# Optimization experiments

Measured on AMD Instinct MI355X. Metric: run time of the kernel, lower is better.

## Reference

```python
import jax, jax.numpy as jnp
import numpy as np

C = 32          # mid_channel / in_channel
B = 8           # batch size (number of scenes)
N = 2_000_000   # total points across batch
BN_EPS = 1e-4   # BatchNorm1d eps from norm_fn


def setup_inputs() -> dict:
    key = jax.random.key(0)
    ks = jax.random.split(key, 8)
    s = 0.05
    return {
        "feats": jax.random.normal(ks[0], (N, C), dtype=jnp.float32),
        "batch_idxs": jnp.sort(jax.random.randint(ks[1], (N,), 0, B, dtype=jnp.int32)),
        "off_w1": jax.random.normal(ks[2], (C, C), dtype=jnp.float32) * s,
        "off_b1": jnp.zeros((C,), jnp.float32),
        "bn_gamma": jnp.ones((C,), jnp.float32),   # set_bn_init fills 1.0
        "bn_beta": jnp.zeros((C,), jnp.float32),   # set_bn_init fills 0.0
        "off_w2": jax.random.normal(ks[3], (C, 3), dtype=jnp.float32) * s,
        "off_b2": jnp.zeros((3,), jnp.float32),
        "mask_w1": jax.random.normal(ks[4], (C, C), dtype=jnp.float32) * s,
        "mask_b1": jnp.zeros((C,), jnp.float32),
        "mask_w2": jax.random.normal(ks[5], (C, 1), dtype=jnp.float32) * s,
        "mask_b2": jnp.zeros((1,), jnp.float32),
        "iou_w": jax.random.normal(ks[6], (C, 1), dtype=jnp.float32) * s,
        "iou_b": jnp.zeros((1,), jnp.float32),
    }


def reference(feats, batch_idxs, off_w1, off_b1, bn_gamma, bn_beta, off_w2, off_b2,
              mask_w1, mask_b1, mask_w2, mask_b2, iou_w, iou_b):
    # offset_linear = MLP([C, C, 3], norm_fn=BatchNorm1d): Linear -> BN -> ReLU -> Linear
    h = feats @ off_w1 + off_b1                      # [N, C]
    mu = h.mean(axis=0)
    var = jnp.mean(jnp.square(h - mu), axis=0)       # biased var (torch BN training fwd)
    h = (h - mu) * jax.lax.rsqrt(var + BN_EPS) * bn_gamma + bn_beta
    h = jax.nn.relu(h)
    pt_offsets = h @ off_w2 + off_b2                 # [N, 3]

    # mask_linear = MLP([C, C, 1], norm_fn=None): Linear -> ReLU -> Linear
    m = jax.nn.relu(feats @ mask_w1 + mask_b1)       # [N, C]
    mask_scores = m @ mask_w2 + mask_b2              # [N, 1]

    # global_pool: scatter mean of features over per-batch segments (batch offsets)
    ones = jnp.ones((feats.shape[0],), feats.dtype)
    counts = jax.ops.segment_sum(ones, batch_idxs, num_segments=B)          # [B]
    pooled = jax.ops.segment_sum(feats, batch_idxs, num_segments=B)         # [B, C]
    pooled = pooled / jnp.maximum(counts, 1.0)[:, None]

    # iou_score_linear on the pooled proposal feature
    iou_scores = pooled @ iou_w + iou_b              # [B, 1]
    return pt_offsets, mask_scores, pooled, iou_scores
```

## Files before the change

kernel.cpp:

```cpp
#include <hip/hip_runtime.h>

#define TPB 256

typedef __attribute__((ext_vector_type(8))) short short8;
typedef __attribute__((ext_vector_type(4))) float floatx4;

__device__ __forceinline__ unsigned short bf_rne(float f){
    union { float f; unsigned u; } c; c.f = f;
    unsigned r = c.u + 0x7fffu + ((c.u >> 16) & 1u);
    return (unsigned short)(r >> 16);
}
__device__ __forceinline__ unsigned pack_bf(float lo, float hi){
    union { float f; unsigned u; } a, b; a.f = lo; b.f = hi;
    return __builtin_amdgcn_perm(b.u, a.u, 0x07060302u);
}

__global__ void lb_kernel(const int* __restrict__ bidx, int* __restrict__ ws_lb,
                          int N, int B)
{
    const int t = threadIdx.x;
    if (t <= B){
        int lo = 0, hi = N;
        while (lo < hi){
            const int mid = (lo + hi) >> 1;
            if (bidx[mid] < t) lo = mid + 1; else hi = mid;
        }
        ws_lb[t] = lo;
    }
}

__global__ __launch_bounds__(TPB) void pass1_kernel(
    const float* __restrict__ feats, const int* __restrict__ ws_lb,
    const float* __restrict__ w1, const float* __restrict__ b1,
    const float* __restrict__ mw1, const float* __restrict__ mb1,
    const float* __restrict__ mw2, const float* __restrict__ mb2,
    float* __restrict__ mask_out,
    float* __restrict__ ws_sum, float* __restrict__ ws_sq,
    float* __restrict__ ws_pool, int N, int B)
{
    __shared__ float s_stage[TPB/64][1024];
    __shared__ float s_pool[8][32];
    __shared__ float s_sum[32];
    __shared__ float s_sq[32];
    __shared__ int   s_lb[9];

    const int tid  = threadIdx.x;
    const int lane = tid & 63;
    const int wv   = tid >> 6;
    const int p = lane & 15;
    const int q = lane >> 4;

    if (tid < 32){ s_sum[tid] = 0.f; s_sq[tid] = 0.f; }
    ((float*)s_pool)[tid] = 0.f;
    if (tid <= B) s_lb[tid] = ws_lb[tid];
    __syncthreads();

    short8 aw0, aw1, am0, am1;
    floatx4 ci_h0, ci_h1, ci_m0, ci_m1;
    float mw2v[8];
#pragma unroll
    for (int j = 0; j < 8; ++j){
        const int k = q * 8 + j;
        aw0[j] = (short)bf_rne(w1 [k * 32 + p]);
        aw1[j] = (short)bf_rne(w1 [k * 32 + 16 + p]);
        am0[j] = (short)bf_rne(mw1[k * 32 + p]);
        am1[j] = (short)bf_rne(mw1[k * 32 + 16 + p]);
    }
#pragma unroll
    for (int r = 0; r < 4; ++r){
        const int c0 = q * 4 + r, c1 = 16 + q * 4 + r;
        ci_h0[r] = b1[c0];  ci_h1[r] = b1[c1];
        ci_m0[r] = mb1[c0]; ci_m1[r] = mb1[c1];
        mw2v[r] = mw2[c0];  mw2v[4 + r] = mw2[c1];
    }
    const float mb2s = mb2[0];

    float hsum[8] = {0,0,0,0,0,0,0,0};
    float hsq [8] = {0,0,0,0,0,0,0,0};
    float pacc[4] = {0,0,0,0};

    const int ngroups = (N + 31) >> 5;
    const int nw  = gridDim.x * (TPB / 64);
    const int wid = blockIdx.x * (TPB / 64) + wv;
    const int g0  = (int)((long)wid       * ngroups / nw);
    const int gE  = (int)((long)(wid + 1) * ngroups / nw);

    int curb = 0;
    { const int r = g0 << 5; while (curb < B - 1 && r >= s_lb[curb + 1]) curb++; }
    int lbn = s_lb[curb + 1];

    float* sw = &s_stage[wv][0];
    const int wrow  = lane >> 3;
    const int wg    = (lane & 7) ^ wrow;
    const int cbase = (lane & 7) << 2;
    const int wo0 = ( 0 + wrow) * 32 + (wg << 2);
    const int wo1 = ( 8 + wrow) * 32 + (wg << 2);
    const int wo2 = (16 + wrow) * 32 + (wg << 2);
    const int wo3 = (24 + wrow) * 32 + (wg << 2);
    const int e = p & 7;
    const int ra0 = p * 32        + ((((q << 1)    ) ^ e) << 2);
    const int ra1 = p * 32        + ((((q << 1) + 1) ^ e) << 2);
    const int rb0 = (16 + p) * 32 + ((((q << 1)    ) ^ e) << 2);
    const int rb1 = (16 + p) * 32 + ((((q << 1) + 1) ^ e) << 2);

    floatx4 sv0 = {0,0,0,0}, sv1 = {0,0,0,0}, sv2 = {0,0,0,0}, sv3 = {0,0,0,0};
    if (g0 < gE){
        const float* gp = feats + ((size_t)g0 << 10) + (lane << 2);
        const int r = (g0 << 5) + wrow;
        if (r + 24 < N){
            sv0 = *(const floatx4*)(gp);
            sv1 = *(const floatx4*)(gp + 256);
            sv2 = *(const floatx4*)(gp + 512);
            sv3 = *(const floatx4*)(gp + 768);
        } else {
            if (r      < N) sv0 = *(const floatx4*)(gp);
            if (r +  8 < N) sv1 = *(const floatx4*)(gp + 256);
            if (r + 16 < N) sv2 = *(const floatx4*)(gp + 512);
            if (r + 24 < N) sv3 = *(const floatx4*)(gp + 768);
        }
    }

    for (int g = g0; g < gE; ++g){
        *(floatx4*)(sw + wo0) = sv0;
        *(floatx4*)(sw + wo1) = sv1;
        *(floatx4*)(sw + wo2) = sv2;
        *(floatx4*)(sw + wo3) = sv3;

        floatx4 nv0 = {0,0,0,0}, nv1 = {0,0,0,0}, nv2 = {0,0,0,0}, nv3 = {0,0,0,0};
        if (g + 1 < gE){
            const float* gp = feats + ((size_t)(g + 1) << 10) + (lane << 2);
            const int r = ((g + 1) << 5) + wrow;
            if (r + 24 < N){
                nv0 = *(const floatx4*)(gp);
                nv1 = *(const floatx4*)(gp + 256);
                nv2 = *(const floatx4*)(gp + 512);
                nv3 = *(const floatx4*)(gp + 768);
            } else {
                if (r      < N) nv0 = *(const floatx4*)(gp);
                if (r +  8 < N) nv1 = *(const floatx4*)(gp + 256);
                if (r + 16 < N) nv2 = *(const floatx4*)(gp + 512);
                if (r + 24 < N) nv3 = *(const floatx4*)(gp + 768);
            }
        }

        const int r0 = g << 5;
        if (r0 >= lbn){
#pragma unroll
            for (int j = 0; j < 4; ++j){
                if (pacc[j] != 0.f) atomicAdd(&s_pool[curb][cbase + j], pacc[j]);
                pacc[j] = 0.f;
            }
            do { curb++; } while (curb < B - 1 && r0 >= s_lb[curb + 1]);
            lbn = s_lb[curb + 1];
        }
        const bool slow = (r0 + 31 >= lbn) || (r0 + 31 >= N);

        if (!slow){
            pacc[0] += sv0[0] + sv1[0] + sv2[0] + sv3[0];
            pacc[1] += sv0[1] + sv1[1] + sv2[1] + sv3[1];
            pacc[2] += sv0[2] + sv1[2] + sv2[2] + sv3[2];
            pacc[3] += sv0[3] + sv1[3] + sv2[3] + sv3[3];
        } else {
#define SLOWROW(SV, L) { \
            const int row = r0 + (L * 8) + wrow; \
            if (row < N){ \
                int bl = curb; \
                for (int c = curb + 1; c < B; ++c) bl += (row >= s_lb[c]); \
                atomicAdd(&s_pool[bl][cbase + 0], SV[0]); \
                atomicAdd(&s_pool[bl][cbase + 1], SV[1]); \
                atomicAdd(&s_pool[bl][cbase + 2], SV[2]); \
                atomicAdd(&s_pool[bl][cbase + 3], SV[3]); \
            } }
            SLOWROW(sv0, 0) SLOWROW(sv1, 1) SLOWROW(sv2, 2) SLOWROW(sv3, 3)
#undef SLOWROW
        }

        const floatx4 vA0 = *(const floatx4*)(sw + ra0);
        const floatx4 vA1 = *(const floatx4*)(sw + ra1);
        const floatx4 vB0 = *(const floatx4*)(sw + rb0);
        const floatx4 vB1 = *(const floatx4*)(sw + rb1);

        short8 bfA, bfB;
        {
            unsigned* ba = (unsigned*)&bfA;
            ba[0] = pack_bf(vA0[0], vA0[1]); ba[1] = pack_bf(vA0[2], vA0[3]);
            ba[2] = pack_bf(vA1[0], vA1[1]); ba[3] = pack_bf(vA1[2], vA1[3]);
            unsigned* bb = (unsigned*)&bfB;
            bb[0] = pack_bf(vB0[0], vB0[1]); bb[1] = pack_bf(vB0[2], vB0[3]);
            bb[2] = pack_bf(vB1[0], vB1[1]); bb[3] = pack_bf(vB1[2], vB1[3]);
        }

        const floatx4 chA0 = __builtin_amdgcn_mfma_f32_16x16x32_bf16(aw0, bfA, ci_h0, 0, 0, 0);
        const floatx4 chA1 = __builtin_amdgcn_mfma_f32_16x16x32_bf16(aw1, bfA, ci_h1, 0, 0, 0);
        const floatx4 cmA0 = __builtin_amdgcn_mfma_f32_16x16x32_bf16(am0, bfA, ci_m0, 0, 0, 0);
        const floatx4 cmA1 = __builtin_amdgcn_mfma_f32_16x16x32_bf16(am1, bfA, ci_m1, 0, 0, 0);
        const floatx4 chB0 = __builtin_amdgcn_mfma_f32_16x16x32_bf16(aw0, bfB, ci_h0, 0, 0, 0);
        const floatx4 chB1 = __builtin_amdgcn_mfma_f32_16x16x32_bf16(aw1, bfB, ci_h1, 0, 0, 0);
        const floatx4 cmB0 = __builtin_amdgcn_mfma_f32_16x16x32_bf16(am0, bfB, ci_m0, 0, 0, 0);
        const floatx4 cmB1 = __builtin_amdgcn_mfma_f32_16x16x32_bf16(am1, bfB, ci_m1, 0, 0, 0);

        if (r0 + 31 < N){
#pragma unroll
            for (int r = 0; r < 4; ++r){
                const float a0 = chA0[r], b0 = chB0[r];
                hsum[r] += a0 + b0;
                hsq [r] = fmaf(a0, a0, fmaf(b0, b0, hsq[r]));
                const float a1 = chA1[r], b1v = chB1[r];
                hsum[4 + r] += a1 + b1v;
                hsq [4 + r] = fmaf(a1, a1, fmaf(b1v, b1v, hsq[4 + r]));
            }
        } else {
            if (r0 + p < N){
#pragma unroll
                for (int r = 0; r < 4; ++r){
                    const float a0 = chA0[r]; hsum[r]     += a0; hsq[r]     = fmaf(a0, a0, hsq[r]);
                    const float a1 = chA1[r]; hsum[4 + r] += a1; hsq[4 + r] = fmaf(a1, a1, hsq[4 + r]);
                }
            }
            if (r0 + 16 + p < N){
#pragma unroll
                for (int r = 0; r < 4; ++r){
                    const float b0 = chB0[r]; hsum[r]     += b0; hsq[r]     = fmaf(b0, b0, hsq[r]);
                    const float b1v = chB1[r]; hsum[4 + r] += b1v; hsq[4 + r] = fmaf(b1v, b1v, hsq[4 + r]);
                }
            }
        }

        float tmA = 0.f, tmB = 0.f;
#pragma unroll
        for (int r = 0; r < 4; ++r){
            tmA = fmaf(fmaxf(cmA0[r], 0.f), mw2v[r],     tmA);
            tmA = fmaf(fmaxf(cmA1[r], 0.f), mw2v[4 + r], tmA);
            tmB = fmaf(fmaxf(cmB0[r], 0.f), mw2v[r],     tmB);
            tmB = fmaf(fmaxf(cmB1[r], 0.f), mw2v[4 + r], tmB);
        }
        tmA += __shfl_xor(tmA, 16, 64); tmA += __shfl_xor(tmA, 32, 64);
        tmB += __shfl_xor(tmB, 16, 64); tmB += __shfl_xor(tmB, 32, 64);
        if (q == 0 && (r0 + p) < N)      mask_out[r0 + p]      = tmA + mb2s;
        if (q == 0 && (r0 + 16 + p) < N) mask_out[r0 + 16 + p] = tmB + mb2s;

        sv0 = nv0; sv1 = nv1; sv2 = nv2; sv3 = nv3;
    }

#pragma unroll
    for (int j = 0; j < 4; ++j){
        if (pacc[j] != 0.f) atomicAdd(&s_pool[curb][cbase + j], pacc[j]);
    }
#pragma unroll
    for (int i = 0; i < 8; ++i){
        const int ch = (i >> 2) * 16 + q * 4 + (i & 3);
        atomicAdd(&s_sum[ch], hsum[i]);
        atomicAdd(&s_sq[ch],  hsq[i]);
    }
    __syncthreads();
    if (tid < 32){
        atomicAdd(&ws_sum[tid], s_sum[tid]);
        atomicAdd(&ws_sq[tid],  s_sq[tid]);
    }
    {
        const float pv = ((float*)s_pool)[tid];
        if (pv != 0.f) atomicAdd(&ws_pool[tid], pv);
    }
}

__global__ __launch_bounds__(TPB) void pass2_kernel(
    const float* __restrict__ feats, const int* __restrict__ ws_lb,
    const float* __restrict__ w1, const float* __restrict__ b1,
    const float* __restrict__ gamma, const float* __restrict__ beta,
    const float* __restrict__ w2, const float* __restrict__ b2,
    const float* __restrict__ iw, const float* __restrict__ ib,
    const float* __restrict__ ws_sum, const float* __restrict__ ws_sq,
    const float* __restrict__ ws_pool,
    float* __restrict__ pt_out, float* __restrict__ pooled_out,
    float* __restrict__ iou_out, int N, int B)
{
    __shared__ float s_stage[TPB/64][1024];
    __shared__ float s_sc[32];
    __shared__ float s_bp[32];
    __shared__ float s_pooled[256];
    __shared__ int   s_lb[9];

    const int tid  = threadIdx.x;
    const int lane = tid & 63;
    const int wv   = tid >> 6;
    const int p = lane & 15;
    const int q = lane >> 4;

    if (tid < 32){
        const float invN = 1.f / (float)N;
        const float mu  = ws_sum[tid] * invN;
        const float var = ws_sq[tid] * invN - mu * mu;
        const float s   = gamma[tid] * rsqrtf(var + 1e-4f);
        s_sc[tid] = s;
        s_bp[tid] = (b1[tid] - mu) * s + beta[tid];
    }
    if (tid <= B) s_lb[tid] = ws_lb[tid];
    __syncthreads();

    if (blockIdx.x == 0){
        if (tid < B * 32){
            const int bb = tid >> 5;
            const float cnt = fmaxf((float)(s_lb[bb + 1] - s_lb[bb]), 1.f);
            const float pv = ws_pool[tid] / cnt;
            s_pooled[tid]   = pv;
            pooled_out[tid] = pv;
        }
        __syncthreads();
        if (tid < B){
            float acc = ib[0];
#pragma unroll
            for (int i = 0; i < 32; ++i) acc = fmaf(s_pooled[tid * 32 + i], iw[i], acc);
            iou_out[tid] = acc;
        }
    }

    short8 pw0, pw1;
    floatx4 pc0, pc1;
    float w2v[24];
    const float sc0 = s_sc[p], sc1 = s_sc[16 + p];
#pragma unroll
    for (int j = 0; j < 8; ++j){
        const int k = q * 8 + j;
        pw0[j] = (short)bf_rne(w1[k * 32 + p]      * sc0);
        pw1[j] = (short)bf_rne(w1[k * 32 + 16 + p] * sc1);
    }
#pragma unroll
    for (int r = 0; r < 4; ++r){
        pc0[r] = s_bp[q * 4 + r];
        pc1[r] = s_bp[16 + q * 4 + r];
    }
#pragma unroll
    for (int i = 0; i < 8; ++i){
        const int ch = (i >> 2) * 16 + q * 4 + (i & 3);
        w2v[i]      = w2[ch * 3 + 0];
        w2v[8 + i]  = w2[ch * 3 + 1];
        w2v[16 + i] = w2[ch * 3 + 2];
    }
    const float b2v0 = b2[0], b2v1 = b2[1], b2v2 = b2[2];

    const int ngroups = (N + 31) >> 5;
    const int nw  = gridDim.x * (TPB / 64);
    const int wid = blockIdx.x * (TPB / 64) + wv;
    const int g0  = (int)((long)wid       * ngroups / nw);
    const int gE  = (int)((long)(wid + 1) * ngroups / nw);

    float* sw = &s_stage[wv][0];
    const int wrow = lane >> 3;
    const int wg   = (lane & 7) ^ wrow;
    const int wo0 = ( 0 + wrow) * 32 + (wg << 2);
    const int wo1 = ( 8 + wrow) * 32 + (wg << 2);
    const int wo2 = (16 + wrow) * 32 + (wg << 2);
    const int wo3 = (24 + wrow) * 32 + (wg << 2);
    const int e = p & 7;
    const int ra0 = p * 32        + ((((q << 1)    ) ^ e) << 2);
    const int ra1 = p * 32        + ((((q << 1) + 1) ^ e) << 2);
    const int rb0 = (16 + p) * 32 + ((((q << 1)    ) ^ e) << 2);
    const int rb1 = (16 + p) * 32 + ((((q << 1) + 1) ^ e) << 2);

    floatx4 sv0 = {0,0,0,0}, sv1 = {0,0,0,0}, sv2 = {0,0,0,0}, sv3 = {0,0,0,0};
    if (g0 < gE){
        const float* gp = feats + ((size_t)g0 << 10) + (lane << 2);
        const int r = (g0 << 5) + wrow;
        if (r + 24 < N){
            sv0 = *(const floatx4*)(gp);
            sv1 = *(const floatx4*)(gp + 256);
            sv2 = *(const floatx4*)(gp + 512);
            sv3 = *(const floatx4*)(gp + 768);
        } else {
            if (r      < N) sv0 = *(const floatx4*)(gp);
            if (r +  8 < N) sv1 = *(const floatx4*)(gp + 256);
            if (r + 16 < N) sv2 = *(const floatx4*)(gp + 512);
            if (r + 24 < N) sv3 = *(const floatx4*)(gp + 768);
        }
    }

    for (int g = g0; g < gE; ++g){
        *(floatx4*)(sw + wo0) = sv0;
        *(floatx4*)(sw + wo1) = sv1;
        *(floatx4*)(sw + wo2) = sv2;
        *(floatx4*)(sw + wo3) = sv3;

        floatx4 nv0 = {0,0,0,0}, nv1 = {0,0,0,0}, nv2 = {0,0,0,0}, nv3 = {0,0,0,0};
        if (g + 1 < gE){
            const float* gp = feats + ((size_t)(g + 1) << 10) + (lane << 2);
            const int r = ((g + 1) << 5) + wrow;
            if (r + 24 < N){
                nv0 = *(const floatx4*)(gp);
                nv1 = *(const floatx4*)(gp + 256);
                nv2 = *(const floatx4*)(gp + 512);
                nv3 = *(const floatx4*)(gp + 768);
            } else {
                if (r      < N) nv0 = *(const floatx4*)(gp);
                if (r +  8 < N) nv1 = *(const floatx4*)(gp + 256);
                if (r + 16 < N) nv2 = *(const floatx4*)(gp + 512);
                if (r + 24 < N) nv3 = *(const floatx4*)(gp + 768);
            }
        }

        const floatx4 vA0 = *(const floatx4*)(sw + ra0);
        const floatx4 vA1 = *(const floatx4*)(sw + ra1);
        const floatx4 vB0 = *(const floatx4*)(sw + rb0);
        const floatx4 vB1 = *(const floatx4*)(sw + rb1);

        short8 bfA, bfB;
        {
            unsigned* ba = (unsigned*)&bfA;
            ba[0] = pack_bf(vA0[0], vA0[1]); ba[1] = pack_bf(vA0[2], vA0[3]);
            ba[2] = pack_bf(vA1[0], vA1[1]); ba[3] = pack_bf(vA1[2], vA1[3]);
            unsigned* bb = (unsigned*)&bfB;
            bb[0] = pack_bf(vB0[0], vB0[1]); bb[1] = pack_bf(vB0[2], vB0[3]);
            bb[2] = pack_bf(vB1[0], vB1[1]); bb[3] = pack_bf(vB1[2], vB1[3]);
        }

        const floatx4 cA0 = __builtin_amdgcn_mfma_f32_16x16x32_bf16(pw0, bfA, pc0, 0, 0, 0);
        const floatx4 cA1 = __builtin_amdgcn_mfma_f32_16x16x32_bf16(pw1, bfA, pc1, 0, 0, 0);
        const floatx4 cB0 = __builtin_amdgcn_mfma_f32_16x16x32_bf16(pw0, bfB, pc0, 0, 0, 0);
        const floatx4 cB1 = __builtin_amdgcn_mfma_f32_16x16x32_bf16(pw1, bfB, pc1, 0, 0, 0);

        float sA0 = 0.f, sA1 = 0.f, sA2 = 0.f, sB0 = 0.f, sB1 = 0.f, sB2 = 0.f;
#pragma unroll
        for (int r = 0; r < 4; ++r){
            const float a0 = fmaxf(cA0[r], 0.f);
            const float a1 = fmaxf(cA1[r], 0.f);
            sA0 = fmaf(a0, w2v[r],      sA0); sA0 = fmaf(a1, w2v[4 + r],  sA0);
            sA1 = fmaf(a0, w2v[8 + r],  sA1); sA1 = fmaf(a1, w2v[12 + r], sA1);
            sA2 = fmaf(a0, w2v[16 + r], sA2); sA2 = fmaf(a1, w2v[20 + r], sA2);
            const float b0 = fmaxf(cB0[r], 0.f);
            const float b1v = fmaxf(cB1[r], 0.f);
            sB0 = fmaf(b0, w2v[r],      sB0); sB0 = fmaf(b1v, w2v[4 + r],  sB0);
            sB1 = fmaf(b0, w2v[8 + r],  sB1); sB1 = fmaf(b1v, w2v[12 + r], sB1);
            sB2 = fmaf(b0, w2v[16 + r], sB2); sB2 = fmaf(b1v, w2v[20 + r], sB2);
        }
        sA0 += __shfl_xor(sA0, 16, 64); sA0 += __shfl_xor(sA0, 32, 64);
        sA1 += __shfl_xor(sA1, 16, 64); sA1 += __shfl_xor(sA1, 32, 64);
        sA2 += __shfl_xor(sA2, 16, 64); sA2 += __shfl_xor(sA2, 32, 64);
        sB0 += __shfl_xor(sB0, 16, 64); sB0 += __shfl_xor(sB0, 32, 64);
        sB1 += __shfl_xor(sB1, 16, 64); sB1 += __shfl_xor(sB1, 32, 64);
        sB2 += __shfl_xor(sB2, 16, 64); sB2 += __shfl_xor(sB2, 32, 64);

        const int r0 = g << 5;
        const int rA = r0 + p, rB = r0 + 16 + p;
        if (lane < 48 && rA < N){
            float val = (q == 0) ? (sA0 + b2v0) : ((q == 1) ? (sA1 + b2v1) : (sA2 + b2v2));
            pt_out[(size_t)rA * 3 + q] = val;
        }
        if (lane < 48 && rB < N){
            float val = (q == 0) ? (sB0 + b2v0) : ((q == 1) ? (sB1 + b2v1) : (sB2 + b2v2));
            pt_out[(size_t)rB * 3 + q] = val;
        }

        sv0 = nv0; sv1 = nv1; sv2 = nv2; sv3 = nv3;
    }
}

extern "C" void kernel_launch(void* const* d_in, const int* in_sizes, int n_in,
                              void* d_out, int out_size, void* d_ws, size_t ws_size,
                              hipStream_t stream) {
    const float* feats = (const float*)d_in[0];
    const int*   bidx  = (const int*)d_in[1];
    const float* w1    = (const float*)d_in[2];
    const float* b1    = (const float*)d_in[3];
    const float* gamma = (const float*)d_in[4];
    const float* beta  = (const float*)d_in[5];
    const float* w2    = (const float*)d_in[6];
    const float* b2    = (const float*)d_in[7];
    const float* mw1   = (const float*)d_in[8];
    const float* mb1   = (const float*)d_in[9];
    const float* mw2   = (const float*)d_in[10];
    const float* mb2   = (const float*)d_in[11];
    const float* iw    = (const float*)d_in[12];
    const float* ib    = (const float*)d_in[13];

    const int N = in_sizes[0] / 32;
    const int B = (out_size - 4 * N) / 33;

    float* out    = (float*)d_out;
    float* pt     = out;
    float* mask   = out + (size_t)3 * N;
    float* pooled = out + (size_t)4 * N;
    float* iou    = pooled + (size_t)B * 32;

    float* ws      = (float*)d_ws;
    float* ws_sum  = ws;
    float* ws_sq   = ws + 32;
    float* ws_pool = ws + 64;
    int*   ws_lb   = (int*)(ws + 64 + (size_t)B * 32);

    hipMemsetAsync(ws, 0, (size_t)(64 + B * 32) * sizeof(float), stream);

    int dev = 0;
    hipGetDevice(&dev);
    hipDeviceProp_t prop;
    hipGetDeviceProperties(&prop, dev);
    int per1 = 0, per2 = 0;
    hipOccupancyMaxActiveBlocksPerMultiprocessor(&per1, pass1_kernel, TPB, 0);
    hipOccupancyMaxActiveBlocksPerMultiprocessor(&per2, pass2_kernel, TPB, 0);
    int g1 = per1 * prop.multiProcessorCount; if (g1 < 512) g1 = 512;
    int g2 = per2 * prop.multiProcessorCount; if (g2 < 512) g2 = 512;

    lb_kernel<<<1, 64, 0, stream>>>(bidx, ws_lb, N, B);
    pass1_kernel<<<g1, TPB, 0, stream>>>(feats, ws_lb, w1, b1, mw1, mb1, mw2, mb2,
                                         mask, ws_sum, ws_sq, ws_pool, N, B);
    pass2_kernel<<<g2, TPB, 0, stream>>>(feats, ws_lb, w1, b1, gamma, beta, w2, b2,
                                         iw, ib, ws_sum, ws_sq, ws_pool,
                                         pt, pooled, iou, N, B);
}
```

Measured before the change: 455.3 us.

## Stream feats directly into LDS with triple-buffered async global_load_lds pipeline

Result: no change. 453.3 us (-0.4%).

```diff
diff --git a/kernel.cpp b/kernel.cpp
--- a/kernel.cpp
+++ b/kernel.cpp
@@ -1,9 +1,13 @@
 #include <hip/hip_runtime.h>
 
 #define TPB 256
+#define GRID_BLOCKS 768
 
 typedef __attribute__((ext_vector_type(8))) short short8;
 typedef __attribute__((ext_vector_type(4))) float floatx4;
+
+typedef __attribute__((address_space(3))) unsigned lds_u32;
+typedef const __attribute__((address_space(1))) unsigned glb_u32;
 
 __device__ __forceinline__ unsigned short bf_rne(float f){
     union { float f; unsigned u; } c; c.f = f;
@@ -14,6 +18,11 @@
     union { float f; unsigned u; } a, b; a.f = lo; b.f = hi;
     return __builtin_amdgcn_perm(b.u, a.u, 0x07060302u);
 }
+__device__ __forceinline__ void gload16(const float* g, float* l){
+    __builtin_amdgcn_global_load_lds((glb_u32*)g, (lds_u32*)l, 16, 0, 0);
+}
+
+#define VMWAIT(n) asm volatile("s_waitcnt vmcnt(" #n ")" ::: "memory")
 
 __global__ void lb_kernel(const int* __restrict__ bidx, int* __restrict__ ws_lb,
                           int N, int B)
@@ -38,7 +47,7 @@
     float* __restrict__ ws_sum, float* __restrict__ ws_sq,
     float* __restrict__ ws_pool, int N, int B)
 {
-    __shared__ float s_stage[TPB/64][1024];
+    __shared__ float s_stage[TPB/64][3072];
     __shared__ float s_pool[8][32];
     __shared__ float s_sum[32];
     __shared__ float s_sq[32];
@@ -90,60 +99,46 @@
     int lbn = s_lb[curb + 1];
 
     float* sw = &s_stage[wv][0];
-    const int wrow  = lane >> 3;
-    const int wg    = (lane & 7) ^ wrow;
-    const int cbase = (lane & 7) << 2;
-    const int wo0 = ( 0 + wrow) * 32 + (wg << 2);
-    const int wo1 = ( 8 + wrow) * 32 + (wg << 2);
-    const int wo2 = (16 + wrow) * 32 + (wg << 2);
-    const int wo3 = (24 + wrow) * 32 + (wg << 2);
+    const int wrow = lane >> 3;
+    const int gofs = ((lane & 7) ^ wrow) << 2;
+    const int cbase = gofs;
+    const int Nm1 = N - 1;
     const int e = p & 7;
     const int ra0 = p * 32        + ((((q << 1)    ) ^ e) << 2);
     const int ra1 = p * 32        + ((((q << 1) + 1) ^ e) << 2);
     const int rb0 = (16 + p) * 32 + ((((q << 1)    ) ^ e) << 2);
     const int rb1 = (16 + p) * 32 + ((((q << 1) + 1) ^ e) << 2);
 
-    floatx4 sv0 = {0,0,0,0}, sv1 = {0,0,0,0}, sv2 = {0,0,0,0}, sv3 = {0,0,0,0};
-    if (g0 < gE){
-        const float* gp = feats + ((size_t)g0 << 10) + (lane << 2);
-        const int r = (g0 << 5) + wrow;
-        if (r + 24 < N){
-            sv0 = *(const floatx4*)(gp);
-            sv1 = *(const floatx4*)(gp + 256);
-            sv2 = *(const floatx4*)(gp + 512);
-            sv3 = *(const floatx4*)(gp + 768);
-        } else {
-            if (r      < N) sv0 = *(const floatx4*)(gp);
-            if (r +  8 < N) sv1 = *(const floatx4*)(gp + 256);
-            if (r + 16 < N) sv2 = *(const floatx4*)(gp + 512);
-            if (r + 24 < N) sv3 = *(const floatx4*)(gp + 768);
-        }
-    }
+#define ISSUE_GROUP(J) { \
+    float* lb_ = sw + ((J) % 3) * 1024; \
+    const int rbase_ = (J) << 5; \
+    _Pragma("unroll") \
+    for (int k_ = 0; k_ < 4; ++k_){ \
+        int row_ = rbase_ + (k_ << 3) + wrow; \
+        row_ = row_ < Nm1 ? row_ : Nm1; \
+        gload16(feats + ((size_t)row_ << 5) + gofs, lb_ + (k_ << 8)); \
+    } }
+
+    int issued = g0;
+    if (issued < gE)          { ISSUE_GROUP(issued); ++issued; }
+    if (issued < gE && issued < g0 + 2){ ISSUE_GROUP(issued); ++issued; }
 
     for (int g = g0; g < gE; ++g){
-        *(floatx4*)(sw + wo0) = sv0;
-        *(floatx4*)(sw + wo1) = sv1;
-        *(floatx4*)(sw + wo2) = sv2;
-        *(floatx4*)(sw + wo3) = sv3;
-
-        floatx4 nv0 = {0,0,0,0}, nv1 = {0,0,0,0}, nv2 = {0,0,0,0}, nv3 = {0,0,0,0};
-        if (g + 1 < gE){
-            const float* gp = feats + ((size_t)(g + 1) << 10) + (lane << 2);
-            const int r = ((g + 1) << 5) + wrow;
-            if (r + 24 < N){
-                nv0 = *(const floatx4*)(gp);
-                nv1 = *(const floatx4*)(gp + 256);
-                nv2 = *(const floatx4*)(gp + 512);
-                nv3 = *(const floatx4*)(gp + 768);
-            } else {
-                if (r      < N) nv0 = *(const floatx4*)(gp);
-                if (r +  8 < N) nv1 = *(const floatx4*)(gp + 256);
-                if (r + 16 < N) nv2 = *(const floatx4*)(gp + 512);
-                if (r + 24 < N) nv3 = *(const floatx4*)(gp + 768);
-            }
-        }
-
+        if (issued < gE){ ISSUE_GROUP(issued); ++issued; }
+        const int ahead = issued - g - 1;
+        if (ahead >= 2)      { VMWAIT(12); }
+        else if (ahead == 1) { VMWAIT(8); }
+        else                 { VMWAIT(0); }
+        __builtin_amdgcn_sched_barrier(0);
+
+        const float* cb = sw + (g % 3) * 1024;
         const int r0 = g << 5;
+
+        const floatx4 pv0 = *(const floatx4*)(cb + (lane << 2));
+        const floatx4 pv1 = *(const floatx4*)(cb + 256 + (lane << 2));
+        const floatx4 pv2 = *(const floatx4*)(cb + 512 + (lane << 2));
+        const floatx4 pv3 = *(const floatx4*)(cb + 768 + (lane << 2));
+
         if (r0 >= lbn){
 #pragma unroll
             for (int j = 0; j < 4; ++j){
@@ -156,10 +151,10 @@
         const bool slow = (r0 + 31 >= lbn) || (r0 + 31 >= N);
 
         if (!slow){
-            pacc[0] += sv0[0] + sv1[0] + sv2[0] + sv3[0];
-            pacc[1] += sv0[1] + sv1[1] + sv2[1] + sv3[1];
-            pacc[2] += sv0[2] + sv1[2] + sv2[2] + sv3[2];
-            pacc[3] += sv0[3] + sv1[3] + sv2[3] + sv3[3];
+            pacc[0] += pv0[0] + pv1[0] + pv2[0] + pv3[0];
+            pacc[1] += pv0[1] + pv1[1] + pv2[1] + pv3[1];
+            pacc[2] += pv0[2] + pv1[2] + pv2[2] + pv3[2];
+            pacc[3] += pv0[3] + pv1[3] + pv2[3] + pv3[3];
         } else {
 #define SLOWROW(SV, L) { \
             const int row = r0 + (L * 8) + wrow; \
@@ -171,14 +166,14 @@
                 atomicAdd(&s_pool[bl][cbase + 2], SV[2]); \
                 atomicAdd(&s_pool[bl][cbase + 3], SV[3]); \
             } }
-            SLOWROW(sv0, 0) SLOWROW(sv1, 1) SLOWROW(sv2, 2) SLOWROW(sv3, 3)
+            SLOWROW(pv0, 0) SLOWROW(pv1, 1) SLOWROW(pv2, 2) SLOWROW(pv3, 3)
 #undef SLOWROW
         }
 
-        const floatx4 vA0 = *(const floatx4*)(sw + ra0);
-        const floatx4 vA1 = *(const floatx4*)(sw + ra1);
-        const floatx4 vB0 = *(const floatx4*)(sw + rb0);
-        const floatx4 vB1 = *(const floatx4*)(sw + rb1);
+        const floatx4 vA0 = *(const floatx4*)(cb + ra0);
+        const floatx4 vA1 = *(const floatx4*)(cb + ra1);
+        const floatx4 vB0 = *(const floatx4*)(cb + rb0);
+        const floatx4 vB1 = *(const floatx4*)(cb + rb1);
 
         short8 bfA, bfB;
         {
@@ -238,8 +233,6 @@
         tmB += __shfl_xor(tmB, 16, 64); tmB += __shfl_xor(tmB, 32, 64);
         if (q == 0 && (r0 + p) < N)      mask_out[r0 + p]      = tmA + mb2s;
         if (q == 0 && (r0 + 16 + p) < N) mask_out[r0 + 16 + p] = tmB + mb2s;
-
-        sv0 = nv0; sv1 = nv1; sv2 = nv2; sv3 = nv3;
     }
 
 #pragma unroll
@@ -261,6 +254,7 @@
         const float pv = ((float*)s_pool)[tid];
         if (pv != 0.f) atomicAdd(&ws_pool[tid], pv);
     }
+#undef ISSUE_GROUP
 }
 
 __global__ __launch_bounds__(TPB) void pass2_kernel(
@@ -274,7 +268,7 @@
     float* __restrict__ pt_out, float* __restrict__ pooled_out,
     float* __restrict__ iou_out, int N, int B)
 {
-    __shared__ float s_stage[TPB/64][1024];
+    __shared__ float s_stage[TPB/64][3072];
     __shared__ float s_sc[32];
     __shared__ float s_bp[32];
     __shared__ float s_pooled[256];
@@ -346,61 +340,42 @@
 
     float* sw = &s_stage[wv][0];
     const int wrow = lane >> 3;
-    const int wg   = (lane & 7) ^ wrow;
-    const int wo0 = ( 0 + wrow) * 32 + (wg << 2);
-    const int wo1 = ( 8 + wrow) * 32 + (wg << 2);
-    const int wo2 = (16 + wrow) * 32 + (wg << 2);
-    const int wo3 = (24 + wrow) * 32 + (wg << 2);
+    const int gofs = ((lane & 7) ^ wrow) << 2;
+    const int Nm1 = N - 1;
     const int e = p & 7;
     const int ra0 = p * 32        + ((((q << 1)    ) ^ e) << 2);
     const int ra1 = p * 32        + ((((q << 1) + 1) ^ e) << 2);
     const int rb0 = (16 + p) * 32 + ((((q << 1)    ) ^ e) << 2);
     const int rb1 = (16 + p) * 32 + ((((q << 1) + 1) ^ e) << 2);
 
-    floatx4 sv0 = {0,0,0,0}, sv1 = {0,0,0,0}, sv2 = {0,0,0,0}, sv3 = {0,0,0,0};
-    if (g0 < gE){
-        const float* gp = feats + ((size_t)g0 << 10) + (lane << 2);
-        const int r = (g0 << 5) + wrow;
-        if (r + 24 < N){
-            sv0 = *(const floatx4*)(gp);
-            sv1 = *(const floatx4*)(gp + 256);
-            sv2 = *(const floatx4*)(gp + 512);
-            sv3 = *(const floatx4*)(gp + 768);
-        } else {
-            if (r      < N) sv0 = *(const floatx4*)(gp);
-            if (r +  8 < N) sv1 = *(const floatx4*)(gp + 256);
-            if (r + 16 < N) sv2 = *(const floatx4*)(gp + 512);
-            if (r + 24 < N) sv3 = *(const floatx4*)(gp + 768);
-        }
-    }
+#define ISSUE_GROUP(J) { \
+    float* lb_ = sw + ((J) % 3) * 1024; \
+    const int rbase_ = (J) << 5; \
+    _Pragma("unroll") \
+    for (int k_ = 0; k_ < 4; ++k_){ \
+        int row_ = rbase_ + (k_ << 3) + wrow; \
+        row_ = row_ < Nm1 ? row_ : Nm1; \
+        gload16(feats + ((size_t)row_ << 5) + gofs, lb_ + (k_ << 8)); \
+    } }
+
+    int issued = g0;
+    if (issued < gE)          { ISSUE_GROUP(issued); ++issued; }
+    if (issued < gE && issued < g0 + 2){ ISSUE_GROUP(issued); ++issued; }
 
     for (int g = g0; g < gE; ++g){
-        *(floatx4*)(sw + wo0) = sv0;
-        *(floatx4*)(sw + wo1) = sv1;
-        *(floatx4*)(sw + wo2) = sv2;
-        *(floatx4*)(sw + wo3) = sv3;
-
-        floatx4 nv0 = {0,0,0,0}, nv1 = {0,0,0,0}, nv2 = {0,0,0,0}, nv3 = {0,0,0,0};
-        if (g + 1 < gE){
-            const float* gp = feats + ((size_t)(g + 1) << 10) + (lane << 2);
-            const int r = ((g + 1) << 5) + wrow;
-            if (r + 24 < N){
-                nv0 = *(const floatx4*)(gp);
-                nv1 = *(const floatx4*)(gp + 256);
-                nv2 = *(const floatx4*)(gp + 512);
-                nv3 = *(const floatx4*)(gp + 768);
-            } else {
-                if (r      < N) nv0 = *(const floatx4*)(gp);
-                if (r +  8 < N) nv1 = *(const floatx4*)(gp + 256);
-                if (r + 16 < N) nv2 = *(const floatx4*)(gp + 512);
-                if (r + 24 < N) nv3 = *(const floatx4*)(gp + 768);
-            }
-        }
-
-        const floatx4 vA0 = *(const floatx4*)(sw + ra0);
-        const floatx4 vA1 = *(const floatx4*)(sw + ra1);
-        const floatx4 vB0 = *(const floatx4*)(sw + rb0);
-        const floatx4 vB1 = *(const floatx4*)(sw + rb1);
+        if (issued < gE){ ISSUE_GROUP(issued); ++issued; }
+        const int ahead = issued - g - 1;
+        if (ahead >= 2)      { VMWAIT(12); }
+        else if (ahead == 1) { VMWAIT(8); }
+        else                 { VMWAIT(0); }
+        __builtin_amdgcn_sched_barrier(0);
+
+        const float* cb = sw + (g % 3) * 1024;
+
+        const floatx4 vA0 = *(const floatx4*)(cb + ra0);
+        const floatx4 vA1 = *(const floatx4*)(cb + ra1);
+        const floatx4 vB0 = *(const floatx4*)(cb + rb0);
+        const floatx4 vB1 = *(const floatx4*)(cb + rb1);
 
         short8 bfA, bfB;
         {
@@ -448,9 +423,8 @@
             float val = (q == 0) ? (sB0 + b2v0) : ((q == 1) ? (sB1 + b2v1) : (sB2 + b2v2));
             pt_out[(size_t)rB * 3 + q] = val;
         }
-
-        sv0 = nv0; sv1 = nv1; sv2 = nv2; sv3 = nv3;
-    }
+    }
+#undef ISSUE_GROUP
 }
 
 extern "C" void kernel_launch(void* const* d_in, const int* in_sizes, int n_in,
@@ -488,20 +462,10 @@
 
     hipMemsetAsync(ws, 0, (size_t)(64 + B * 32) * sizeof(float), stream);
 
-    int dev = 0;
-    hipGetDevice(&dev);
-    hipDeviceProp_t prop;
-    hipGetDeviceProperties(&prop, dev);
-    int per1 = 0, per2 = 0;
-    hipOccupancyMaxActiveBlocksPerMultiprocessor(&per1, pass1_kernel, TPB, 0);
-    hipOccupancyMaxActiveBlocksPerMultiprocessor(&per2, pass2_kernel, TPB, 0);
-    int g1 = per1 * prop.multiProcessorCount; if (g1 < 512) g1 = 512;
-    int g2 = per2 * prop.multiProcessorCount; if (g2 < 512) g2 = 512;
-
     lb_kernel<<<1, 64, 0, stream>>>(bidx, ws_lb, N, B);
-    pass1_kernel<<<g1, TPB, 0, stream>>>(feats, ws_lb, w1, b1, mw1, mb1, mw2, mb2,
-                                         mask, ws_sum, ws_sq, ws_pool, N, B);
-    pass2_kernel<<<g2, TPB, 0, stream>>>(feats, ws_lb, w1, b1, gamma, beta, w2, b2,
-                                         iw, ib, ws_sum, ws_sq, ws_pool,
-                                         pt, pooled, iou, N, B);
-}
+    pass1_kernel<<<GRID_BLOCKS, TPB, 0, stream>>>(feats, ws_lb, w1, b1, mw1, mb1, mw2, mb2,
+                                                  mask, ws_sum, ws_sq, ws_pool, N, B);
+    pass2_kernel<<<GRID_BLOCKS, TPB, 0, stream>>>(feats, ws_lb, w1, b1, gamma, beta, w2, b2,
+                                                  iw, ib, ws_sum, ws_sq, ws_pool,
+                                                  pt, pooled, iou, N, B);
+}
```

## Store pre-BN hidden activations in fp16 and make pass2 a lightweight elementwise head

Applied to the files above, without the earlier changes.

Result: no change. 462.5 us (+1.6%).

```diff
diff --git a/kernel.cpp b/kernel.cpp
--- a/kernel.cpp
+++ b/kernel.cpp
@@ -1,6 +1,8 @@
 #include <hip/hip_runtime.h>
 
 #define TPB 256
+#define GRID1 1024
+#define GRID2 2048
 
 typedef __attribute__((ext_vector_type(8))) short short8;
 typedef __attribute__((ext_vector_type(4))) float floatx4;
@@ -13,6 +15,15 @@
 __device__ __forceinline__ unsigned pack_bf(float lo, float hi){
     union { float f; unsigned u; } a, b; a.f = lo; b.f = hi;
     return __builtin_amdgcn_perm(b.u, a.u, 0x07060302u);
+}
+__device__ __forceinline__ unsigned short f2h(float a){
+    union { _Float16 f; unsigned short u; } c; c.f = (_Float16)a; return c.u;
+}
+__device__ __forceinline__ unsigned pk16(float a, float b){
+    return (unsigned)f2h(a) | ((unsigned)f2h(b) << 16);
+}
+__device__ __forceinline__ float h2f(unsigned short u){
+    union { unsigned short u; _Float16 f; } c; c.u = u; return (float)c.f;
 }
 
 __global__ void lb_kernel(const int* __restrict__ bidx, int* __restrict__ ws_lb,
@@ -34,7 +45,7 @@
     const float* __restrict__ w1, const float* __restrict__ b1,
     const float* __restrict__ mw1, const float* __restrict__ mb1,
     const float* __restrict__ mw2, const float* __restrict__ mb2,
-    float* __restrict__ mask_out,
+    float* __restrict__ mask_out, unsigned short* __restrict__ h_out,
     float* __restrict__ ws_sum, float* __restrict__ ws_sq,
     float* __restrict__ ws_pool, int N, int B)
 {
@@ -199,6 +210,24 @@
         const floatx4 cmB0 = __builtin_amdgcn_mfma_f32_16x16x32_bf16(am0, bfB, ci_m0, 0, 0, 0);
         const floatx4 cmB1 = __builtin_amdgcn_mfma_f32_16x16x32_bf16(am1, bfB, ci_m1, 0, 0, 0);
 
+        {
+            const int rA = r0 + p, rB = r0 + 16 + p;
+            if (rA < N){
+                uint2 wlo, whi;
+                wlo.x = pk16(chA0[0], chA0[1]); wlo.y = pk16(chA0[2], chA0[3]);
+                whi.x = pk16(chA1[0], chA1[1]); whi.y = pk16(chA1[2], chA1[3]);
+                *(uint2*)(h_out + (size_t)rA * 32 + q * 4)      = wlo;
+                *(uint2*)(h_out + (size_t)rA * 32 + 16 + q * 4) = whi;
+            }
+            if (rB < N){
+                uint2 wlo, whi;
+                wlo.x = pk16(chB0[0], chB0[1]); wlo.y = pk16(chB0[2], chB0[3]);
+                whi.x = pk16(chB1[0], chB1[1]); whi.y = pk16(chB1[2], chB1[3]);
+                *(uint2*)(h_out + (size_t)rB * 32 + q * 4)      = wlo;
+                *(uint2*)(h_out + (size_t)rB * 32 + 16 + q * 4) = whi;
+            }
+        }
+
         if (r0 + 31 < N){
 #pragma unroll
             for (int r = 0; r < 4; ++r){
@@ -264,8 +293,7 @@
 }
 
 __global__ __launch_bounds__(TPB) void pass2_kernel(
-    const float* __restrict__ feats, const int* __restrict__ ws_lb,
-    const float* __restrict__ w1, const float* __restrict__ b1,
+    const unsigned short* __restrict__ h_in, const int* __restrict__ ws_lb,
     const float* __restrict__ gamma, const float* __restrict__ beta,
     const float* __restrict__ w2, const float* __restrict__ b2,
     const float* __restrict__ iw, const float* __restrict__ ib,
@@ -274,17 +302,12 @@
     float* __restrict__ pt_out, float* __restrict__ pooled_out,
     float* __restrict__ iou_out, int N, int B)
 {
-    __shared__ float s_stage[TPB/64][1024];
     __shared__ float s_sc[32];
     __shared__ float s_bp[32];
     __shared__ float s_pooled[256];
     __shared__ int   s_lb[9];
 
-    const int tid  = threadIdx.x;
-    const int lane = tid & 63;
-    const int wv   = tid >> 6;
-    const int p = lane & 15;
-    const int q = lane >> 4;
+    const int tid = threadIdx.x;
 
     if (tid < 32){
         const float invN = 1.f / (float)N;
@@ -292,7 +315,7 @@
         const float var = ws_sq[tid] * invN - mu * mu;
         const float s   = gamma[tid] * rsqrtf(var + 1e-4f);
         s_sc[tid] = s;
-        s_bp[tid] = (b1[tid] - mu) * s + beta[tid];
+        s_bp[tid] = beta[tid] - mu * s;
     }
     if (tid <= B) s_lb[tid] = ws_lb[tid];
     __syncthreads();
@@ -314,142 +337,37 @@
         }
     }
 
-    short8 pw0, pw1;
-    floatx4 pc0, pc1;
-    float w2v[24];
-    const float sc0 = s_sc[p], sc1 = s_sc[16 + p];
+    const int q4 = tid & 3;
+    float sc[8], bp[8], wv0[8], wv1[8], wv2[8];
 #pragma unroll
     for (int j = 0; j < 8; ++j){
-        const int k = q * 8 + j;
-        pw0[j] = (short)bf_rne(w1[k * 32 + p]      * sc0);
-        pw1[j] = (short)bf_rne(w1[k * 32 + 16 + p] * sc1);
-    }
-#pragma unroll
-    for (int r = 0; r < 4; ++r){
-        pc0[r] = s_bp[q * 4 + r];
-        pc1[r] = s_bp[16 + q * 4 + r];
-    }
-#pragma unroll
-    for (int i = 0; i < 8; ++i){
-        const int ch = (i >> 2) * 16 + q * 4 + (i & 3);
-        w2v[i]      = w2[ch * 3 + 0];
-        w2v[8 + i]  = w2[ch * 3 + 1];
-        w2v[16 + i] = w2[ch * 3 + 2];
-    }
-    const float b2v0 = b2[0], b2v1 = b2[1], b2v2 = b2[2];
-
-    const int ngroups = (N + 31) >> 5;
-    const int nw  = gridDim.x * (TPB / 64);
-    const int wid = blockIdx.x * (TPB / 64) + wv;
-    const int g0  = (int)((long)wid       * ngroups / nw);
-    const int gE  = (int)((long)(wid + 1) * ngroups / nw);
-
-    float* sw = &s_stage[wv][0];
-    const int wrow = lane >> 3;
-    const int wg   = (lane & 7) ^ wrow;
-    const int wo0 = ( 0 + wrow) * 32 + (wg << 2);
-    const int wo1 = ( 8 + wrow) * 32 + (wg << 2);
-    const int wo2 = (16 + wrow) * 32 + (wg << 2);
-    const int wo3 = (24 + wrow) * 32 + (wg << 2);
-    const int e = p & 7;
-    const int ra0 = p * 32        + ((((q << 1)    ) ^ e) << 2);
-    const int ra1 = p * 32        + ((((q << 1) + 1) ^ e) << 2);
-    const int rb0 = (16 + p) * 32 + ((((q << 1)    ) ^ e) << 2);
-    const int rb1 = (16 + p) * 32 + ((((q << 1) + 1) ^ e) << 2);
-
-    floatx4 sv0 = {0,0,0,0}, sv1 = {0,0,0,0}, sv2 = {0,0,0,0}, sv3 = {0,0,0,0};
-    if (g0 < gE){
-        const float* gp = feats + ((size_t)g0 << 10) + (lane << 2);
-        const int r = (g0 << 5) + wrow;
-        if (r + 24 < N){
-            sv0 = *(const floatx4*)(gp);
-            sv1 = *(const floatx4*)(gp + 256);
-            sv2 = *(const floatx4*)(gp + 512);
-            sv3 = *(const floatx4*)(gp + 768);
-        } else {
-            if (r      < N) sv0 = *(const floatx4*)(gp);
-            if (r +  8 < N) sv1 = *(const floatx4*)(gp + 256);
-            if (r + 16 < N) sv2 = *(const floatx4*)(gp + 512);
-            if (r + 24 < N) sv3 = *(const floatx4*)(gp + 768);
-        }
-    }
-
-    for (int g = g0; g < gE; ++g){
-        *(floatx4*)(sw + wo0) = sv0;
-        *(floatx4*)(sw + wo1) = sv1;
-        *(floatx4*)(sw + wo2) = sv2;
-        *(floatx4*)(sw + wo3) = sv3;
-
-        floatx4 nv0 = {0,0,0,0}, nv1 = {0,0,0,0}, nv2 = {0,0,0,0}, nv3 = {0,0,0,0};
-        if (g + 1 < gE){
-            const float* gp = feats + ((size_t)(g + 1) << 10) + (lane << 2);
-            const int r = ((g + 1) << 5) + wrow;
-            if (r + 24 < N){
-                nv0 = *(const floatx4*)(gp);
-                nv1 = *(const floatx4*)(gp + 256);
-                nv2 = *(const floatx4*)(gp + 512);
-                nv3 = *(const floatx4*)(gp + 768);
-            } else {
-                if (r      < N) nv0 = *(const floatx4*)(gp);
-                if (r +  8 < N) nv1 = *(const floatx4*)(gp + 256);
-                if (r + 16 < N) nv2 = *(const floatx4*)(gp + 512);
-                if (r + 24 < N) nv3 = *(const floatx4*)(gp + 768);
-            }
-        }
-
-        const floatx4 vA0 = *(const floatx4*)(sw + ra0);
-        const floatx4 vA1 = *(const floatx4*)(sw + ra1);
-        const floatx4 vB0 = *(const floatx4*)(sw + rb0);
-        const floatx4 vB1 = *(const floatx4*)(sw + rb1);
-
-        short8 bfA, bfB;
-        {
-            unsigned* ba = (unsigned*)&bfA;
-            ba[0] = pack_bf(vA0[0], vA0[1]); ba[1] = pack_bf(vA0[2], vA0[3]);
-            ba[2] = pack_bf(vA1[0], vA1[1]); ba[3] = pack_bf(vA1[2], vA1[3]);
-            unsigned* bb = (unsigned*)&bfB;
-            bb[0] = pack_bf(vB0[0], vB0[1]); bb[1] = pack_bf(vB0[2], vB0[3]);
-            bb[2] = pack_bf(vB1[0], vB1[1]); bb[3] = pack_bf(vB1[2], vB1[3]);
-        }
-
-        const floatx4 cA0 = __builtin_amdgcn_mfma_f32_16x16x32_bf16(pw0, bfA, pc0, 0, 0, 0);
-        const floatx4 cA1 = __builtin_amdgcn_mfma_f32_16x16x32_bf16(pw1, bfA, pc1, 0, 0, 0);
-        const floatx4 cB0 = __builtin_amdgcn_mfma_f32_16x16x32_bf16(pw0, bfB, pc0, 0, 0, 0);
-        const floatx4 cB1 = __builtin_amdgcn_mfma_f32_16x16x32_bf16(pw1, bfB, pc1, 0, 0, 0);
-
-        float sA0 = 0.f, sA1 = 0.f, sA2 = 0.f, sB0 = 0.f, sB1 = 0.f, sB2 = 0.f;
-#pragma unroll
-        for (int r = 0; r < 4; ++r){
-            const float a0 = fmaxf(cA0[r], 0.f);
-            const float a1 = fmaxf(cA1[r], 0.f);
-            sA0 = fmaf(a0, w2v[r],      sA0); sA0 = fmaf(a1, w2v[4 + r],  sA0);
-            sA1 = fmaf(a0, w2v[8 + r],  sA1); sA1 = fmaf(a1, w2v[12 + r], sA1);
-            sA2 = fmaf(a0, w2v[16 + r], sA2); sA2 = fmaf(a1, w2v[20 + r], sA2);
-            const float b0 = fmaxf(cB0[r], 0.f);
-            const float b1v = fmaxf(cB1[r], 0.f);
-            sB0 = fmaf(b0, w2v[r],      sB0); sB0 = fmaf(b1v, w2v[4 + r],  sB0);
-            sB1 = fmaf(b0, w2v[8 + r],  sB1); sB1 = fmaf(b1v, w2v[12 + r], sB1);
-            sB2 = fmaf(b0, w2v[16 + r], sB2); sB2 = fmaf(b1v, w2v[20 + r], sB2);
-        }
-        sA0 += __shfl_xor(sA0, 16, 64); sA0 += __shfl_xor(sA0, 32, 64);
-        sA1 += __shfl_xor(sA1, 16, 64); sA1 += __shfl_xor(sA1, 32, 64);
-        sA2 += __shfl_xor(sA2, 16, 64); sA2 += __shfl_xor(sA2, 32, 64);
-        sB0 += __shfl_xor(sB0, 16, 64); sB0 += __shfl_xor(sB0, 32, 64);
-        sB1 += __shfl_xor(sB1, 16, 64); sB1 += __shfl_xor(sB1, 32, 64);
-        sB2 += __shfl_xor(sB2, 16, 64); sB2 += __shfl_xor(sB2, 32, 64);
-
-        const int r0 = g << 5;
-        const int rA = r0 + p, rB = r0 + 16 + p;
-        if (lane < 48 && rA < N){
-            float val = (q == 0) ? (sA0 + b2v0) : ((q == 1) ? (sA1 + b2v1) : (sA2 + b2v2));
-            pt_out[(size_t)rA * 3 + q] = val;
-        }
-        if (lane < 48 && rB < N){
-            float val = (q == 0) ? (sB0 + b2v0) : ((q == 1) ? (sB1 + b2v1) : (sB2 + b2v2));
-            pt_out[(size_t)rB * 3 + q] = val;
-        }
-
-        sv0 = nv0; sv1 = nv1; sv2 = nv2; sv3 = nv3;
+        const int ch = q4 * 8 + j;
+        sc[j]  = s_sc[ch];
+        bp[j]  = s_bp[ch];
+        wv0[j] = w2[ch * 3 + 0];
+        wv1[j] = w2[ch * 3 + 1];
+        wv2[j] = w2[ch * 3 + 2];
+    }
+    const float b2v = (q4 == 0) ? b2[0] : ((q4 == 1) ? b2[1] : b2[2]);
+
+    const int stride = gridDim.x * (TPB / 4);
+    for (int row = blockIdx.x * (TPB / 4) + (tid >> 2); row < N; row += stride){
+        const short8 hv = *(const short8*)(h_in + (size_t)row * 32 + q4 * 8);
+        float d0 = 0.f, d1 = 0.f, d2 = 0.f;
+#pragma unroll
+        for (int j = 0; j < 8; ++j){
+            const float x = fmaxf(fmaf(h2f((unsigned short)hv[j]), sc[j], bp[j]), 0.f);
+            d0 = fmaf(x, wv0[j], d0);
+            d1 = fmaf(x, wv1[j], d1);
+            d2 = fmaf(x, wv2[j], d2);
+        }
+        d0 += __shfl_xor(d0, 1, 64); d0 += __shfl_xor(d0, 2, 64);
+        d1 += __shfl_xor(d1, 1, 64); d1 += __shfl_xor(d1, 2, 64);
+        d2 += __shfl_xor(d2, 1, 64); d2 += __shfl_xor(d2, 2, 64);
+        if (q4 < 3){
+            const float val = (q4 == 0) ? d0 : ((q4 == 1) ? d1 : d2);
+            pt_out[(size_t)row * 3 + q4] = val + b2v;
+        }
     }
 }
 
@@ -485,23 +403,14 @@
     float* ws_sq   = ws + 32;
     float* ws_pool = ws + 64;
     int*   ws_lb   = (int*)(ws + 64 + (size_t)B * 32);
-
-    hipMemsetAsync(ws, 0, (size_t)(64 + B * 32) * sizeof(float), stream);
-
-    int dev = 0;
-    hipGetDevice(&dev);
-    hipDeviceProp_t prop;
-    hipGetDeviceProperties(&prop, dev);
-    int per1 = 0, per2 = 0;
-    hipOccupancyMaxActiveBlocksPerMultiprocessor(&per1, pass1_kernel, TPB, 0);
-    hipOccupancyMaxActiveBlocksPerMultiprocessor(&per2, pass2_kernel, TPB, 0);
-    int g1 = per1 * prop.multiProcessorCount; if (g1 < 512) g1 = 512;
-    int g2 = per2 * prop.multiProcessorCount; if (g2 < 512) g2 = 512;
+    unsigned short* ws_h = (unsigned short*)(ws + 384);
+
+    (void)hipMemsetAsync(ws, 0, (size_t)(64 + B * 32) * sizeof(float), stream);
 
     lb_kernel<<<1, 64, 0, stream>>>(bidx, ws_lb, N, B);
-    pass1_kernel<<<g1, TPB, 0, stream>>>(feats, ws_lb, w1, b1, mw1, mb1, mw2, mb2,
-                                         mask, ws_sum, ws_sq, ws_pool, N, B);
-    pass2_kernel<<<g2, TPB, 0, stream>>>(feats, ws_lb, w1, b1, gamma, beta, w2, b2,
-                                         iw, ib, ws_sum, ws_sq, ws_pool,
-                                         pt, pooled, iou, N, B);
-}
+    pass1_kernel<<<GRID1, TPB, 0, stream>>>(feats, ws_lb, w1, b1, mw1, mb1, mw2, mb2,
+                                            mask, ws_h, ws_sum, ws_sq, ws_pool, N, B);
+    pass2_kernel<<<GRID2, TPB, 0, stream>>>(ws_h, ws_lb, gamma, beta, w2, b2,
+                                            iw, ib, ws_sum, ws_sq, ws_pool,
+                                            pt, pooled, iou, N, B);
+}
```
